# Performance work log

Measured on AMD Instinct MI355X. Metric: run time of the kernel, lower is better.

The kernel has to match this reference:

```python
import jax, jax.numpy as jnp
import numpy as np

N = 2097152          # total proposals
C = 21               # classes (0 = background)
NUM_CLUSTERS = 4096
IGNORE_INDEX = -1
EPS = 1e-12          # numerical guard on log, as custom CUDA loss kernels do


def setup_inputs() -> dict:
    key = jax.random.key(0)
    k1, k2, k3, k4, k5 = jax.random.split(key, 5)
    input_ = jax.random.uniform(k1, (N, C), dtype=jnp.float32)
    weight = jax.random.uniform(k2, (N,), dtype=jnp.float32)
    pc_input = jax.random.uniform(k3, (NUM_CLUSTERS,), dtype=jnp.float32)
    target = jax.random.randint(k4, (N,), 0, C, dtype=jnp.int64 if jax.config.jax_enable_x64 else jnp.int32)
    cluster = jax.random.randint(k5, (N,), 0, NUM_CLUSTERS, dtype=jnp.int64 if jax.config.jax_enable_x64 else jnp.int32)
    return {"input": input_, "weight": weight, "pc_input": pc_input,
            "target": target, "cluster": cluster}


def reference(input, weight, pc_input, target, cluster):
    # PCL loss, reduction='mean', ignore_index=-1
    valid = target != IGNORE_INDEX                      # [N] bool
    is_bg = target == 0                                 # [N] bool
    # background proposals: own prob of class 0; foreground: cluster-averaged prob
    p_fg = pc_input[cluster]                            # irregular gather [N]
    p = jnp.where(is_bg, input[:, 0], p_fg)             # [N]
    per_sample = -weight * jnp.log(jnp.maximum(p, EPS))
    per_sample = jnp.where(valid, per_sample, 0.0)
    n_valid = jnp.maximum(valid.sum().astype(per_sample.dtype), 1.0)
    return per_sample.sum() / n_valid
```

## Files before the change

kernel.cpp:

```cpp
#include <hip/hip_runtime.h>
#include <cmath>

#define C_CLASSES 21
#define EPS 1e-12f
#define IGNORE_INDEX (-1)

struct PclWs {
    double sum;
    unsigned int cnt;
    unsigned int pad;
};

__global__ __launch_bounds__(256) void pcl_reduce_kernel(
    const float* __restrict__ input,
    const float* __restrict__ weight,
    const float* __restrict__ pc_input,
    const int*   __restrict__ target,
    const int*   __restrict__ cluster,
    PclWs* __restrict__ ws,
    int n)
{
    const int tid  = blockIdx.x * blockDim.x + threadIdx.x;
    const int base = tid * 4;

    float lsum = 0.0f;
    int   lcnt = 0;

    if (base + 3 < n) {
        const int4   t4 = *reinterpret_cast<const int4*>(target + base);
        const int4   c4 = *reinterpret_cast<const int4*>(cluster + base);
        const float4 w4 = *reinterpret_cast<const float4*>(weight + base);

        const int   ts[4] = {t4.x, t4.y, t4.z, t4.w};
        const int   cs[4] = {c4.x, c4.y, c4.z, c4.w};
        const float wv[4] = {w4.x, w4.y, w4.z, w4.w};

#pragma unroll
        for (int j = 0; j < 4; ++j) {
            const int t = ts[j];
            if (t == IGNORE_INDEX) continue;
            ++lcnt;
            float p;
            if (t == 0) {
                p = input[(size_t)(base + j) * C_CLASSES];
            } else {
                p = pc_input[cs[j]];
            }
            lsum += -wv[j] * logf(fmaxf(p, EPS));
        }
    } else if (base < n) {
        for (int j = 0; j < 4 && base + j < n; ++j) {
            const int i = base + j;
            const int t = target[i];
            if (t == IGNORE_INDEX) continue;
            ++lcnt;
            float p = (t == 0) ? input[(size_t)i * C_CLASSES]
                               : pc_input[cluster[i]];
            lsum += -weight[i] * logf(fmaxf(p, EPS));
        }
    }

#pragma unroll
    for (int off = 32; off > 0; off >>= 1) {
        lsum += __shfl_down(lsum, off, 64);
        lcnt += __shfl_down(lcnt, off, 64);
    }

    __shared__ float ssum[4];
    __shared__ int   scnt[4];
    const int wave = threadIdx.x >> 6;
    const int lane = threadIdx.x & 63;
    if (lane == 0) { ssum[wave] = lsum; scnt[wave] = lcnt; }
    __syncthreads();

    if (threadIdx.x == 0) {
        float bs = ssum[0] + ssum[1] + ssum[2] + ssum[3];
        int   bc = scnt[0] + scnt[1] + scnt[2] + scnt[3];
        atomicAdd(&ws->sum, (double)bs);
        atomicAdd(&ws->cnt, (unsigned int)bc);
    }
}

__global__ void pcl_finalize_kernel(const PclWs* __restrict__ ws,
                                    float* __restrict__ out)
{
    double denom = (double)ws->cnt;
    if (denom < 1.0) denom = 1.0;
    out[0] = (float)(ws->sum / denom);
}

extern "C" void kernel_launch(void* const* d_in, const int* in_sizes, int n_in,
                              void* d_out, int out_size, void* d_ws, size_t ws_size,
                              hipStream_t stream) {
    const float* input    = (const float*)d_in[0];
    const float* weight   = (const float*)d_in[1];
    const float* pc_input = (const float*)d_in[2];
    const int*   target   = (const int*)d_in[3];
    const int*   cluster  = (const int*)d_in[4];
    float* out = (float*)d_out;
    PclWs* ws  = (PclWs*)d_ws;

    const int n = in_sizes[1];

    hipMemsetAsync(ws, 0, sizeof(PclWs), stream);

    const int threads = 256;
    const int groups  = (n + 3) / 4;
    const int blocks  = (groups + threads - 1) / threads;

    pcl_reduce_kernel<<<blocks, threads, 0, stream>>>(
        input, weight, pc_input, target, cluster, ws, n);

    pcl_finalize_kernel<<<1, 1, 0, stream>>>(ws, out);
}
```

Measured before the change: 274.2 us.

## Replace global atomics with per-block partials and a parallel finalize reduction

```diff
diff --git a/kernel.cpp b/kernel.cpp
--- a/kernel.cpp
+++ b/kernel.cpp
@@ -4,39 +4,40 @@
 #define C_CLASSES 21
 #define EPS 1e-12f
 #define IGNORE_INDEX (-1)
+#define THREADS 256
+#define EPT 8
 
-struct PclWs {
-    double sum;
-    unsigned int cnt;
-    unsigned int pad;
-};
 
-__global__ __launch_bounds__(256) void pcl_reduce_kernel(
+__global__ __launch_bounds__(THREADS) void pcl_reduce_kernel(
     const float* __restrict__ input,
     const float* __restrict__ weight,
     const float* __restrict__ pc_input,
     const int*   __restrict__ target,
     const int*   __restrict__ cluster,
-    PclWs* __restrict__ ws,
+    float* __restrict__ part_sum,
+    int*   __restrict__ part_cnt,
     int n)
 {
-    const int tid  = blockIdx.x * blockDim.x + threadIdx.x;
-    const int base = tid * 4;
+    const int tid  = blockIdx.x * THREADS + threadIdx.x;
+    const int base = tid * EPT;
 
     float lsum = 0.0f;
     int   lcnt = 0;
 
-    if (base + 3 < n) {
-        const int4   t4 = *reinterpret_cast<const int4*>(target + base);
-        const int4   c4 = *reinterpret_cast<const int4*>(cluster + base);
-        const float4 w4 = *reinterpret_cast<const float4*>(weight + base);
+    if (base + EPT - 1 < n) {
+        const int4   t0 = *reinterpret_cast<const int4*>(target + base);
+        const int4   t1 = *reinterpret_cast<const int4*>(target + base + 4);
+        const int4   c0 = *reinterpret_cast<const int4*>(cluster + base);
+        const int4   c1 = *reinterpret_cast<const int4*>(cluster + base + 4);
+        const float4 w0 = *reinterpret_cast<const float4*>(weight + base);
+        const float4 w1 = *reinterpret_cast<const float4*>(weight + base + 4);
 
-        const int   ts[4] = {t4.x, t4.y, t4.z, t4.w};
-        const int   cs[4] = {c4.x, c4.y, c4.z, c4.w};
-        const float wv[4] = {w4.x, w4.y, w4.z, w4.w};
+        const int   ts[EPT] = {t0.x, t0.y, t0.z, t0.w, t1.x, t1.y, t1.z, t1.w};
+        const int   cs[EPT] = {c0.x, c0.y, c0.z, c0.w, c1.x, c1.y, c1.z, c1.w};
+        const float wv[EPT] = {w0.x, w0.y, w0.z, w0.w, w1.x, w1.y, w1.z, w1.w};
 
 #pragma unroll
-        for (int j = 0; j < 4; ++j) {
+        for (int j = 0; j < EPT; ++j) {
             const int t = ts[j];
             if (t == IGNORE_INDEX) continue;
             ++lcnt;
@@ -46,17 +47,17 @@
             } else {
                 p = pc_input[cs[j]];
             }
-            lsum += -wv[j] * logf(fmaxf(p, EPS));
+            lsum -= wv[j] * logf(fmaxf(p, EPS));
         }
     } else if (base < n) {
-        for (int j = 0; j < 4 && base + j < n; ++j) {
+        for (int j = 0; j < EPT && base + j < n; ++j) {
             const int i = base + j;
             const int t = target[i];
             if (t == IGNORE_INDEX) continue;
             ++lcnt;
             float p = (t == 0) ? input[(size_t)i * C_CLASSES]
                                : pc_input[cluster[i]];
-            lsum += -weight[i] * logf(fmaxf(p, EPS));
+            lsum -= weight[i] * logf(fmaxf(p, EPS));
         }
     }
 
@@ -66,27 +67,53 @@
         lcnt += __shfl_down(lcnt, off, 64);
     }
 
-    __shared__ float ssum[4];
-    __shared__ int   scnt[4];
+    __shared__ float ssum[THREADS / 64];
+    __shared__ int   scnt[THREADS / 64];
     const int wave = threadIdx.x >> 6;
     const int lane = threadIdx.x & 63;
     if (lane == 0) { ssum[wave] = lsum; scnt[wave] = lcnt; }
     __syncthreads();
 
     if (threadIdx.x == 0) {
-        float bs = ssum[0] + ssum[1] + ssum[2] + ssum[3];
-        int   bc = scnt[0] + scnt[1] + scnt[2] + scnt[3];
-        atomicAdd(&ws->sum, (double)bs);
-        atomicAdd(&ws->cnt, (unsigned int)bc);
+        float bs = 0.0f; int bc = 0;
+#pragma unroll
+        for (int w = 0; w < THREADS / 64; ++w) { bs += ssum[w]; bc += scnt[w]; }
+        part_sum[blockIdx.x] = bs;
+        part_cnt[blockIdx.x] = bc;
     }
 }
 
-__global__ void pcl_finalize_kernel(const PclWs* __restrict__ ws,
-                                    float* __restrict__ out)
+__global__ __launch_bounds__(THREADS) void pcl_finalize_kernel(
+    const float* __restrict__ part_sum,
+    const int*   __restrict__ part_cnt,
+    float* __restrict__ out,
+    int nblocks)
 {
-    double denom = (double)ws->cnt;
-    if (denom < 1.0) denom = 1.0;
-    out[0] = (float)(ws->sum / denom);
+    double lsum = 0.0;
+    long long lcnt = 0;
+    for (int i = threadIdx.x; i < nblocks; i += THREADS) {
+        lsum += (double)part_sum[i];
+        lcnt += part_cnt[i];
+    }
+#pragma unroll
+    for (int off = 32; off > 0; off >>= 1) {
+        lsum += __shfl_down(lsum, off, 64);
+        lcnt += __shfl_down(lcnt, off, 64);
+    }
+    __shared__ double ssum[THREADS / 64];
+    __shared__ long long scnt[THREADS / 64];
+    const int wave = threadIdx.x >> 6;
+    const int lane = threadIdx.x & 63;
+    if (lane == 0) { ssum[wave] = lsum; scnt[wave] = lcnt; }
+    __syncthreads();
+    if (threadIdx.x == 0) {
+        double s = 0.0; long long c = 0;
+#pragma unroll
+        for (int w = 0; w < THREADS / 64; ++w) { s += ssum[w]; c += scnt[w]; }
+        double denom = (double)c;
+        if (denom < 1.0) denom = 1.0;
+        out[0] = (float)(s / denom);
+    }
 }
 
 extern "C" void kernel_launch(void* const* d_in, const int* in_sizes, int n_in,
@@ -98,18 +125,17 @@
     const int*   target   = (const int*)d_in[3];
     const int*   cluster  = (const int*)d_in[4];
     float* out = (float*)d_out;
-    PclWs* ws  = (PclWs*)d_ws;
 
     const int n = in_sizes[1];
 
-    hipMemsetAsync(ws, 0, sizeof(PclWs), stream);
+    const int groups = (n + EPT - 1) / EPT;
+    const int blocks = (groups + THREADS - 1) / THREADS;
 
-    const int threads = 256;
-    const int groups  = (n + 3) / 4;
-    const int blocks  = (groups + threads - 1) / threads;
+    float* part_sum = (float*)d_ws;
+    int*   part_cnt = (int*)((char*)d_ws + (size_t)blocks * sizeof(float));
 
-    pcl_reduce_kernel<<<blocks, threads, 0, stream>>>(
-        input, weight, pc_input, target, cluster, ws, n);
+    pcl_reduce_kernel<<<blocks, THREADS, 0, stream>>>(
+        input, weight, pc_input, target, cluster, part_sum, part_cnt, n);
 
-    pcl_finalize_kernel<<<1, 1, 0, stream>>>(ws, out);
+    pcl_finalize_kernel<<<1, THREADS, 0, stream>>>(part_sum, part_cnt, out, blocks);
 }
```

Measured after the change: 230.6 us. 15.9% less time.
